# Optimization experiments

Hardware: AMD Instinct MI355X
Metric: run time of the kernel (lower is better)

The kernel has to match this reference:

```python
import jax, jax.numpy as jnp
from jax import lax
import numpy as np

B, CIN, COUT, H, W = 32, 64, 64, 128, 128
KH = KW = 1
STRIDE = (1, 1)
PADDING = ((0, 0), (0, 0))


def setup_inputs() -> dict:
    key = jax.random.key(0)
    k1, k2, k3, k4 = jax.random.split(key, 4)
    x_quant = jax.random.randint(k1, (B, CIN, H, W), 0, 256, dtype=jnp.int32)  # uint8 values
    weight_int8 = jax.random.randint(k2, (COUT, CIN, KH, KW), -127, 128, dtype=jnp.int32)
    weight_scale = jax.random.uniform(k3, (COUT, 1, 1, 1), dtype=jnp.float32, minval=0.001, maxval=0.02)
    weight_zero_point = jnp.zeros((COUT, 1, 1, 1), dtype=jnp.int32)
    bias_fp32 = jax.random.normal(k4, (COUT,), dtype=jnp.float32) * 0.1
    return {
        "x_quant": x_quant,
        "input_scale": jnp.float32(0.02),
        "input_zero_point": jnp.int32(128),
        "weight_int8": weight_int8,
        "weight_scale": weight_scale,
        "weight_zero_point": weight_zero_point,
        "bias_fp32": bias_fp32,
        "output_scale": jnp.float32(0.05),
        "output_zero_point": jnp.int32(128),
    }


def reference(x_quant, input_scale, input_zero_point, weight_int8, weight_scale,
              weight_zero_point, bias_fp32, output_scale, output_zero_point):
    # dequant (zero-point subtract) in fp32
    x = x_quant.astype(jnp.float32) - input_zero_point.astype(jnp.float32)          # [B,Cin,H,W]
    w = weight_int8.astype(jnp.float32) - weight_zero_point.astype(jnp.float32)     # [O,I,kh,kw]
    conv = lax.conv_general_dilated(
        x, w, window_strides=STRIDE, padding=PADDING,
        dimension_numbers=("NCHW", "OIHW", "NCHW"))                                 # [B,O,H',W']
    # requantize: per-out-channel scale + bias, round, clamp to uint8 range
    requant_scale = (input_scale * weight_scale / output_scale).reshape(1, COUT, 1, 1)
    bias_term = (bias_fp32 / output_scale).reshape(1, COUT, 1, 1)
    final_float = conv * requant_scale + bias_term
    requant = jnp.round(final_float) + output_zero_point.astype(jnp.float32)
    out_q = jnp.clip(requant, 0.0, 255.0).astype(jnp.uint8)
    return out_q
```

## Files before the change

### kernel.cpp

```cpp
#include <hip/hip_runtime.h>

#define CIN   64
#define COUT  64
#define HW    16384
#define PXB   128
#define NPIX  (32 * HW)

__global__ void prep_kernel(const int* __restrict__ w,
                            const float* __restrict__ wscale,
                            const int* __restrict__ wzp,
                            const float* __restrict__ bias,
                            const float* __restrict__ is_p,
                            const float* __restrict__ os_p,
                            const int* __restrict__ ozp_p,
                            int* __restrict__ wp,
                            float4* __restrict__ params) {
    int o = threadIdx.x;
    if (o >= COUT) return;
    int zp = wzp[o];
    int sum = 0;
    #pragma unroll
    for (int k = 0; k < 16; ++k) {
        int c0 = w[o * CIN + 4 * k + 0] - zp;
        int c1 = w[o * CIN + 4 * k + 1] - zp;
        int c2 = w[o * CIN + 4 * k + 2] - zp;
        int c3 = w[o * CIN + 4 * k + 3] - zp;
        sum += c0 + c1 + c2 + c3;
        wp[o * 16 + k] = (c0 & 0xff) | ((c1 & 0xff) << 8) |
                         ((c2 & 0xff) << 16) | ((c3 & 0xff) << 24);
    }
    float scale = is_p[0] * wscale[o] / os_p[0];
    float bterm = bias[o] / os_p[0] + (float)ozp_p[0];
    float4 pr;
    pr.x = scale;
    pr.y = bterm;
    pr.z = __int_as_float(sum);
    pr.w = 0.0f;
    params[o] = pr;
}

__global__ __launch_bounds__(128) void conv_kernel(
    const int* __restrict__ x,
    const int* __restrict__ wp_g,
    const float4* __restrict__ params_g,
    const int* __restrict__ izp_p,
    int* __restrict__ out) {

    __shared__ int    s_x[CIN * PXB];
    __shared__ int4   s_wp[COUT * 4];
    __shared__ float4 s_par[COUT];

    const int tid  = threadIdx.x;
    const int wave = tid >> 6;
    const int lane = tid & 63;

    const int t0 = blockIdx.x * PXB;
    const int b  = t0 >> 14;
    const int p0 = t0 & (HW - 1);
    const int* xb = x + b * (CIN * HW) + p0;

    #pragma unroll
    for (int j = 0; j < 16; ++j) {
        const int c  = (wave * 16 + j) * 2;
        const int cl = c + (lane >> 5);
        const int* gp = xb + cl * HW + (lane & 31) * 4;
        __builtin_amdgcn_global_load_lds(
            (const __attribute__((address_space(1))) int*)gp,
            (__attribute__((address_space(3))) int*)&s_x[c * PXB],
            16, 0, 0);
    }

    s_wp[tid]       = ((const int4*)wp_g)[tid];
    s_wp[tid + 128] = ((const int4*)wp_g)[tid + 128];
    if (tid < COUT) s_par[tid] = params_g[tid];
    const int izp_adj = izp_p[0] - 128;

    __syncthreads();

    int px[16];
    #pragma unroll
    for (int cg = 0; cg < 16; ++cg) {
        int v0 = s_x[(4 * cg + 0) * PXB + tid];
        int v1 = s_x[(4 * cg + 1) * PXB + tid];
        int v2 = s_x[(4 * cg + 2) * PXB + tid];
        int v3 = s_x[(4 * cg + 3) * PXB + tid];
        px[cg] = (v0 | (v1 << 8) | (v2 << 16) | (v3 << 24)) ^ 0x80808080;
    }

    int* ob = out + b * (COUT * HW) + p0 + tid;

    #pragma unroll 8
    for (int o = 0; o < COUT; ++o) {
        int4 w0 = s_wp[o * 4 + 0];
        int4 w1 = s_wp[o * 4 + 1];
        int4 w2 = s_wp[o * 4 + 2];
        int4 w3 = s_wp[o * 4 + 3];
        float4 pr = s_par[o];
        int wsum = __float_as_int(pr.z);
        int acc = -izp_adj * wsum;

        acc = __builtin_amdgcn_sdot4(px[0],  w0.x, acc, false);
        acc = __builtin_amdgcn_sdot4(px[1],  w0.y, acc, false);
        acc = __builtin_amdgcn_sdot4(px[2],  w0.z, acc, false);
        acc = __builtin_amdgcn_sdot4(px[3],  w0.w, acc, false);
        acc = __builtin_amdgcn_sdot4(px[4],  w1.x, acc, false);
        acc = __builtin_amdgcn_sdot4(px[5],  w1.y, acc, false);
        acc = __builtin_amdgcn_sdot4(px[6],  w1.z, acc, false);
        acc = __builtin_amdgcn_sdot4(px[7],  w1.w, acc, false);
        acc = __builtin_amdgcn_sdot4(px[8],  w2.x, acc, false);
        acc = __builtin_amdgcn_sdot4(px[9],  w2.y, acc, false);
        acc = __builtin_amdgcn_sdot4(px[10], w2.z, acc, false);
        acc = __builtin_amdgcn_sdot4(px[11], w2.w, acc, false);
        acc = __builtin_amdgcn_sdot4(px[12], w3.x, acc, false);
        acc = __builtin_amdgcn_sdot4(px[13], w3.y, acc, false);
        acc = __builtin_amdgcn_sdot4(px[14], w3.z, acc, false);
        acc = __builtin_amdgcn_sdot4(px[15], w3.w, acc, false);

        float f = fmaf((float)acc, pr.x, pr.y);
        f = rintf(f);
        f = fminf(fmaxf(f, 0.0f), 255.0f);
        __builtin_nontemporal_store((int)f, ob + o * HW);
    }
}

extern "C" void kernel_launch(void* const* d_in, const int* in_sizes, int n_in,
                              void* d_out, int out_size, void* d_ws, size_t ws_size,
                              hipStream_t stream) {
    const int*   x      = (const int*)d_in[0];
    const float* is_p   = (const float*)d_in[1];
    const int*   izp_p  = (const int*)d_in[2];
    const int*   w      = (const int*)d_in[3];
    const float* wscale = (const float*)d_in[4];
    const int*   wzp    = (const int*)d_in[5];
    const float* bias   = (const float*)d_in[6];
    const float* os_p   = (const float*)d_in[7];
    const int*   ozp_p  = (const int*)d_in[8];

    int* out = (int*)d_out;

    int*    wp     = (int*)d_ws;
    float4* params = (float4*)((char*)d_ws + 4096);

    prep_kernel<<<1, 64, 0, stream>>>(w, wscale, wzp, bias, is_p, os_p, ozp_p, wp, params);

    conv_kernel<<<4096, 128, 0, stream>>>(x, wp, params, izp_p, out);
}
```

Baseline: 253.9 us.

## Double-buffer input tiles in LDS across a persistent per-block pixel span

Each block now owns a span of 8 tiles of 256 pixels within one image. It prefetches the next tile into a second LDS buffer with global_load_lds while computing the current one, using vmcnt waits and barriers. The grid shrinks from 4096 blocks of 128 threads to 256 blocks of 256 threads, and the weight and param staging happens once per block instead of once per tile. The aim is to overlap input loads with the dot-product and store work. The cost is that the 128KB LDS footprint allows only one block (4 waves) per CU, so much less latency hiding comes from occupancy.

```diff
diff --git a/kernel.cpp b/kernel.cpp
--- a/kernel.cpp
+++ b/kernel.cpp
@@ -3,8 +3,9 @@
 #define CIN   64
 #define COUT  64
 #define HW    16384
-#define PXB   128
-#define NPIX  (32 * HW)
+#define TPX   256
+#define NTILE 8
+#define SPAN  (TPX * NTILE)
 
 __global__ void prep_kernel(const int* __restrict__ w,
                             const float* __restrict__ wscale,
@@ -39,14 +40,14 @@
     params[o] = pr;
 }
 
-__global__ __launch_bounds__(128) void conv_kernel(
+__global__ __launch_bounds__(256) void conv_kernel(
     const int* __restrict__ x,
     const int* __restrict__ wp_g,
     const float4* __restrict__ params_g,
     const int* __restrict__ izp_p,
     int* __restrict__ out) {
 
-    __shared__ int    s_x[CIN * PXB];
+    __shared__ int    s_x[2][CIN * TPX];
     __shared__ int4   s_wp[COUT * 4];
     __shared__ float4 s_par[COUT];
 
@@ -54,73 +55,94 @@
     const int wave = tid >> 6;
     const int lane = tid & 63;
 
-    const int t0 = blockIdx.x * PXB;
-    const int b  = t0 >> 14;
-    const int p0 = t0 & (HW - 1);
-    const int* xb = x + b * (CIN * HW) + p0;
+    const int span   = blockIdx.x;
+    const int b      = span >> 3;
+    const int p_base = (span & 7) * SPAN;
 
-    #pragma unroll
-    for (int j = 0; j < 16; ++j) {
-        const int c  = (wave * 16 + j) * 2;
-        const int cl = c + (lane >> 5);
-        const int* gp = xb + cl * HW + (lane & 31) * 4;
-        __builtin_amdgcn_global_load_lds(
-            (const __attribute__((address_space(1))) int*)gp,
-            (__attribute__((address_space(3))) int*)&s_x[c * PXB],
-            16, 0, 0);
-    }
+    const int* xb      = x   + b * (CIN  * HW);
+    int*       ob_base = out + b * (COUT * HW);
 
-    s_wp[tid]       = ((const int4*)wp_g)[tid];
-    s_wp[tid + 128] = ((const int4*)wp_g)[tid + 128];
+    s_wp[tid] = ((const int4*)wp_g)[tid];
     if (tid < COUT) s_par[tid] = params_g[tid];
     const int izp_adj = izp_p[0] - 128;
-
     __syncthreads();
 
-    int px[16];
-    #pragma unroll
-    for (int cg = 0; cg < 16; ++cg) {
-        int v0 = s_x[(4 * cg + 0) * PXB + tid];
-        int v1 = s_x[(4 * cg + 1) * PXB + tid];
-        int v2 = s_x[(4 * cg + 2) * PXB + tid];
-        int v3 = s_x[(4 * cg + 3) * PXB + tid];
-        px[cg] = (v0 | (v1 << 8) | (v2 << 16) | (v3 << 24)) ^ 0x80808080;
+    auto STAGE = [&](int t, int bi) {
+        const int p0 = p_base + t * TPX;
+        #pragma unroll
+        for (int j = 0; j < 16; ++j) {
+            const int c = wave * 16 + j;
+            const int* gp = xb + c * HW + p0 + lane * 4;
+            __builtin_amdgcn_global_load_lds(
+                (const __attribute__((address_space(1))) int*)gp,
+                (__attribute__((address_space(3))) int*)&s_x[bi][c * TPX],
+                16, 0, 0);
+        }
+    };
+
+    auto COMPUTE = [&](int t, int bi) {
+        const int p0 = p_base + t * TPX;
+        const int* sx = s_x[bi];
+
+        int px[16];
+        #pragma unroll
+        for (int cg = 0; cg < 16; ++cg) {
+            int v0 = sx[(4 * cg + 0) * TPX + tid];
+            int v1 = sx[(4 * cg + 1) * TPX + tid];
+            int v2 = sx[(4 * cg + 2) * TPX + tid];
+            int v3 = sx[(4 * cg + 3) * TPX + tid];
+            px[cg] = (v0 | (v1 << 8) | (v2 << 16) | (v3 << 24)) ^ 0x80808080;
+        }
+
+        int* ob = ob_base + p0 + tid;
+        #pragma unroll 8
+        for (int o = 0; o < COUT; ++o) {
+            int4 w0 = s_wp[o * 4 + 0];
+            int4 w1 = s_wp[o * 4 + 1];
+            int4 w2 = s_wp[o * 4 + 2];
+            int4 w3 = s_wp[o * 4 + 3];
+            float4 pr = s_par[o];
+            int wsum = __float_as_int(pr.z);
+            int acc = -izp_adj * wsum;
+
+            acc = __builtin_amdgcn_sdot4(px[0],  w0.x, acc, false);
+            acc = __builtin_amdgcn_sdot4(px[1],  w0.y, acc, false);
+            acc = __builtin_amdgcn_sdot4(px[2],  w0.z, acc, false);
+            acc = __builtin_amdgcn_sdot4(px[3],  w0.w, acc, false);
+            acc = __builtin_amdgcn_sdot4(px[4],  w1.x, acc, false);
+            acc = __builtin_amdgcn_sdot4(px[5],  w1.y, acc, false);
+            acc = __builtin_amdgcn_sdot4(px[6],  w1.z, acc, false);
+            acc = __builtin_amdgcn_sdot4(px[7],  w1.w, acc, false);
+            acc = __builtin_amdgcn_sdot4(px[8],  w2.x, acc, false);
+            acc = __builtin_amdgcn_sdot4(px[9],  w2.y, acc, false);
+            acc = __builtin_amdgcn_sdot4(px[10], w2.z, acc, false);
+            acc = __builtin_amdgcn_sdot4(px[11], w2.w, acc, false);
+            acc = __builtin_amdgcn_sdot4(px[12], w3.x, acc, false);
+            acc = __builtin_amdgcn_sdot4(px[13], w3.y, acc, false);
+            acc = __builtin_amdgcn_sdot4(px[14], w3.z, acc, false);
+            acc = __builtin_amdgcn_sdot4(px[15], w3.w, acc, false);
+
+            float f = fmaf((float)acc, pr.x, pr.y);
+            f = rintf(f);
+            f = fminf(fmaxf(f, 0.0f), 255.0f);
+            __builtin_nontemporal_store((int)f, ob + o * HW);
+        }
+    };
+
+    STAGE(0, 0);
+    #pragma unroll 1
+    for (int t = 0; t < NTILE - 1; ++t) {
+        STAGE(t + 1, (t + 1) & 1);
+        asm volatile("s_waitcnt vmcnt(16)" ::: "memory");
+        __builtin_amdgcn_s_barrier();
+        __builtin_amdgcn_sched_barrier(0);
+        COMPUTE(t, t & 1);
+        __builtin_amdgcn_s_barrier();
     }
-
-    int* ob = out + b * (COUT * HW) + p0 + tid;
-
-    #pragma unroll 8
-    for (int o = 0; o < COUT; ++o) {
-        int4 w0 = s_wp[o * 4 + 0];
-        int4 w1 = s_wp[o * 4 + 1];
-        int4 w2 = s_wp[o * 4 + 2];
-        int4 w3 = s_wp[o * 4 + 3];
-        float4 pr = s_par[o];
-        int wsum = __float_as_int(pr.z);
-        int acc = -izp_adj * wsum;
-
-        acc = __builtin_amdgcn_sdot4(px[0],  w0.x, acc, false);
-        acc = __builtin_amdgcn_sdot4(px[1],  w0.y, acc, false);
-        acc = __builtin_amdgcn_sdot4(px[2],  w0.z, acc, false);
-        acc = __builtin_amdgcn_sdot4(px[3],  w0.w, acc, false);
-        acc = __builtin_amdgcn_sdot4(px[4],  w1.x, acc, false);
-        acc = __builtin_amdgcn_sdot4(px[5],  w1.y, acc, false);
-        acc = __builtin_amdgcn_sdot4(px[6],  w1.z, acc, false);
-        acc = __builtin_amdgcn_sdot4(px[7],  w1.w, acc, false);
-        acc = __builtin_amdgcn_sdot4(px[8],  w2.x, acc, false);
-        acc = __builtin_amdgcn_sdot4(px[9],  w2.y, acc, false);
-        acc = __builtin_amdgcn_sdot4(px[10], w2.z, acc, false);
-        acc = __builtin_amdgcn_sdot4(px[11], w2.w, acc, false);
-        acc = __builtin_amdgcn_sdot4(px[12], w3.x, acc, false);
-        acc = __builtin_amdgcn_sdot4(px[13], w3.y, acc, false);
-        acc = __builtin_amdgcn_sdot4(px[14], w3.z, acc, false);
-        acc = __builtin_amdgcn_sdot4(px[15], w3.w, acc, false);
-
-        float f = fmaf((float)acc, pr.x, pr.y);
-        f = rintf(f);
-        f = fminf(fmaxf(f, 0.0f), 255.0f);
-        __builtin_nontemporal_store((int)f, ob + o * HW);
-    }
+    asm volatile("s_waitcnt vmcnt(0)" ::: "memory");
+    __builtin_amdgcn_s_barrier();
+    __builtin_amdgcn_sched_barrier(0);
+    COMPUTE(NTILE - 1, (NTILE - 1) & 1);
 }
 
 extern "C" void kernel_launch(void* const* d_in, const int* in_sizes, int n_in,
@@ -143,5 +165,5 @@
 
     prep_kernel<<<1, 64, 0, stream>>>(w, wscale, wzp, bias, is_p, os_p, ozp_p, wp, params);
 
-    conv_kernel<<<4096, 128, 0, stream>>>(x, wp, params, izp_p, out);
+    conv_kernel<<<256, 256, 0, stream>>>(x, wp, params, izp_p, out);
 }
```

Result: slower. 282.2 us (+11.1%).
